# Optimization experiments

Hardware: AMD Instinct MI355X
Metric: run time of the kernel (lower is better)

The kernel has to match this reference:

```python
import jax, jax.numpy as jnp
import numpy as np

B, N, NVT, HS, NZ = 512, 256, 32, 128, 64


def setup_inputs() -> dict:
    key = jax.random.key(0)
    ks = jax.random.split(key, 16)
    node_types = jax.random.randint(ks[0], (B, N), 0, NVT, dtype=jnp.int32)
    node_types = node_types.at[:, 0].set(0)      # START_TYPE
    node_types = node_types.at[:, -1].set(1)     # END_TYPE
    adj = jax.random.randint(ks[1], (B, N, N), 0, 2, dtype=jnp.int32)
    # DAG: edges only u -> v with u < v (strict upper triangular)
    tri = jnp.triu(jnp.ones((N, N), jnp.int32), k=1)
    adj = adj * tri[None, :, :]
    s = 0.05
    p = lambda k, shp: (jax.random.normal(k, shp, jnp.float32) * s)
    return {
        "node_types": node_types,
        "adj": adj,
        "W_ih": p(ks[2], (3 * HS, NVT)),   # grue_forward weight_ih
        "W_hh": p(ks[3], (3 * HS, HS)),    # grue_forward weight_hh
        "b_ih": p(ks[4], (3 * HS,)),
        "b_hh": p(ks[5], (3 * HS,)),
        "Wg": p(ks[6], (HS, NVT)),         # gate_forward linear
        "bg": p(ks[7], (HS,)),
        "Wm": p(ks[8], (HS, NVT)),         # mapper_forward (no bias)
        "W1": p(ks[9], (NZ, HS)),          # fc1 -> mu
        "b1": p(ks[10], (NZ,)),
        "W2": p(ks[11], (NZ, HS)),         # fc2 -> logvar
        "b2": p(ks[12], (NZ,)),
    }


def reference(node_types, adj, W_ih, W_hh, b_ih, b_hh, Wg, bg, Wm, W1, b1, W2, b2):
    hs = Wg.shape[0]
    # one-hot vertex types  [B, N, nvt]
    X = jax.nn.one_hot(node_types, Wg.shape[1], dtype=W_ih.dtype)
    # gated message from each vertex's TYPE (mapper has no bias -> padding contributes 0)
    gated = jax.nn.sigmoid(jnp.einsum('bnv,hv->bnh', X, Wg) + bg) \
            * jnp.einsum('bnv,hv->bnh', X, Wm)                      # [B, N, hs]
    A = adj.astype(gated.dtype)
    # predecessor aggregation: H_v = sum_{u: u->v} gated_u
    Hpre = jnp.einsum('buv,buh->bvh', A, gated)                     # [B, N, hs]
    # torch GRUCell(X_v, Hpre_v), vectorized over all vertices (no recurrence:
    # messages depend only on predecessor types)
    gi = jnp.einsum('bnv,gv->bng', X, W_ih) + b_ih                  # [B, N, 3hs]
    gh = jnp.einsum('bnh,gh->bng', Hpre, W_hh) + b_hh
    r = jax.nn.sigmoid(gi[..., :hs] + gh[..., :hs])
    z = jax.nn.sigmoid(gi[..., hs:2 * hs] + gh[..., hs:2 * hs])
    n = jnp.tanh(gi[..., 2 * hs:] + r * gh[..., 2 * hs:])
    Hv = (1.0 - z) * n + z * Hpre                                   # H_forward, [B, N, hs]
    # graph state: sum over vertices [1, N-1) (start=1, end_offset=1)
    Hg = Hv[:, 1:-1, :].sum(axis=1)                                 # [B, hs]
    mu = Hg @ W1.T + b1
    logvar = Hg @ W2.T + b2
    return (mu, logvar)
```

## Files before the change

### kernel.cpp

```cpp
#include <hip/hip_runtime.h>
#include <hip/hip_bf16.h>

#define HS 128
#define NVT 32
#define NN 256

typedef __attribute__((ext_vector_type(8))) short bf16x8;
typedef __attribute__((ext_vector_type(4))) short s16x4;
typedef __attribute__((ext_vector_type(4))) float f32x4;

#define TABB_OFF 0
#define GIT2_OFF 32768

static __device__ __forceinline__ short f2bs(float f) {
    __hip_bfloat16 h = __float2bfloat16(f);
    short s; __builtin_memcpy(&s, &h, 2);
    return s;
}
static __device__ __forceinline__ float bs2f(short s) {
    __hip_bfloat16 h; __builtin_memcpy(&h, &s, 2);
    return __bfloat162float(h);
}
static __device__ __forceinline__ float sigm(float x) {
    return __builtin_amdgcn_rcpf(1.f + __expf(-x));
}

__global__ void __launch_bounds__(512) build_tables(
    const float* __restrict__ W_ih, const float* __restrict__ W_hh,
    const float* __restrict__ b_ih, const float* __restrict__ b_hh,
    const float* __restrict__ Wg,   const float* __restrict__ bg,
    const float* __restrict__ Wm,
    short* __restrict__ TABB, short* __restrict__ GIT2)
{
    __shared__ float G_s[HS];
    const int t = blockIdx.x;
    const int j = threadIdx.x;
    if (j < HS) {
        float x = Wg[j * NVT + t] + bg[j];
        G_s[j] = sigm(x) * Wm[j * NVT + t];
    }
    __syncthreads();
    if (j < 384) {
        float acc = 0.f;
        for (int h = 0; h < HS; ++h) acc += G_s[h] * W_hh[j * HS + h];
        TABB[j * NVT + t] = f2bs(acc);
        float git = W_ih[j * NVT + t] + b_ih[j];
        int gate = j >> 7, h = j & 127;
        if (gate < 2) git += b_hh[j];
        GIT2[(t * 128 + h) * 4 + gate] = f2bs(git);
    } else {
        TABB[j * NVT + t] = f2bs(G_s[j - 384]);
        GIT2[(t * 128 + (j - 384)) * 4 + 3] = 0;
    }
}

__global__ void __launch_bounds__(256) dvae_fused(
    const int* __restrict__ node_types, const int* __restrict__ adj,
    const short* __restrict__ TABB, const short* __restrict__ GIT2,
    const float* __restrict__ b_hh,
    const float* __restrict__ W1, const float* __restrict__ b1,
    const float* __restrict__ W2, const float* __restrict__ b2,
    float* __restrict__ out)
{
    __shared__ unsigned cntA[NN * 20];
    __shared__ short GITs[NVT * 512];
    __shared__ unsigned pc[4 * NN * 8];
    __shared__ unsigned tmask[NVT * 8];
    __shared__ int types_s[NN];
    __shared__ float hg_s[HS];

    const int b = blockIdx.x, tid = threadIdx.x;
    const int wave = tid >> 6, lane = tid & 63;
    const int quad = lane >> 4, col = lane & 15;

    types_s[tid] = node_types[b * NN + tid];

    {
        const uint4* src = (const uint4*)GIT2;
        uint4* dst = (uint4*)GITs;
        #pragma unroll
        for (int i = 0; i < 8; ++i) dst[i * 256 + tid] = src[i * 256 + tid];
    }
    bf16x8 bfrag[8];
    #pragma unroll
    for (int i = 0; i < 8; ++i) {
        int gate = i >> 1, sub = (i & 1) * 16;
        int jb = (gate < 3 ? gate * 128 : 384) + wave * 32 + sub;
        bfrag[i] = *(const bf16x8*)(TABB + (jb + col) * 32 + quad * 8);
    }
    const int h0 = wave * 32 + col;
    const float bhn0 = b_hh[256 + h0], bhn1 = b_hh[256 + h0 + 16];
    __syncthreads();

    {
        int t = tid >> 3, w8 = tid & 7;
        const int* ty = types_s + w8 * 32;
        unsigned mw = 0;
        #pragma unroll
        for (int k = 0; k < 32; ++k) mw |= ((unsigned)(ty[k] == t)) << k;
        tmask[tid] = mw;
    }

    const uint4* adjb = (const uint4*)(adj + (size_t)b * NN * NN) + wave * 64 * 64 + lane;
    unsigned cb0a = 0, cb0b = 0, cb1a = 0, cb1b = 0, cb2a = 0, cb2b = 0, cb3a = 0, cb3b = 0;
    #pragma unroll
    for (int half = 0; half < 2; ++half) {
        #pragma unroll
        for (int bb = 0; bb < 4; ++bb) {
            uint4 av[8];
            #pragma unroll
            for (int j = 0; j < 8; ++j) av[j] = adjb[(half * 32 + bb * 8 + j) * 64];
            #pragma unroll
            for (int j = 0; j < 8; ++j) {
                int sh = bb * 8 + j;
                if (half == 0) {
                    cb0a |= av[j].x << sh; cb1a |= av[j].y << sh;
                    cb2a |= av[j].z << sh; cb3a |= av[j].w << sh;
                } else {
                    cb0b |= av[j].x << sh; cb1b |= av[j].y << sh;
                    cb2b |= av[j].z << sh; cb3b |= av[j].w << sh;
                }
            }
        }
    }
    __syncthreads();

    unsigned pcnt[4][8];
    #pragma unroll
    for (int k = 0; k < 4; ++k)
        #pragma unroll
        for (int q = 0; q < 8; ++q) pcnt[k][q] = 0;
    #pragma unroll
    for (int t = 0; t < 32; ++t) {
        unsigned tm0 = tmask[t * 8 + wave * 2];
        unsigned tm1 = tmask[t * 8 + wave * 2 + 1];
        unsigned sh = (unsigned)((t & 3) * 8);
        pcnt[0][t >> 2] += (__popc(cb0a & tm0) + __popc(cb0b & tm1)) << sh;
        pcnt[1][t >> 2] += (__popc(cb1a & tm0) + __popc(cb1b & tm1)) << sh;
        pcnt[2][t >> 2] += (__popc(cb2a & tm0) + __popc(cb2b & tm1)) << sh;
        pcnt[3][t >> 2] += (__popc(cb3a & tm0) + __popc(cb3b & tm1)) << sh;
    }
    {
        uint4* p4 = (uint4*)pc;
        #pragma unroll
        for (int k = 0; k < 4; ++k) {
            int c = lane * 4 + k;
            p4[(wave * NN + c) * 2]     = make_uint4(pcnt[k][0], pcnt[k][1], pcnt[k][2], pcnt[k][3]);
            p4[(wave * NN + c) * 2 + 1] = make_uint4(pcnt[k][4], pcnt[k][5], pcnt[k][6], pcnt[k][7]);
        }
    }
    __syncthreads();

    {
        #pragma unroll
        for (int q = 0; q < 8; ++q) {
            unsigned u = pc[(0 * NN + tid) * 8 + q] + pc[(1 * NN + tid) * 8 + q]
                       + pc[(2 * NN + tid) * 8 + q] + pc[(3 * NN + tid) * 8 + q];
            float f0 = (float)(u & 0xFF),         f1 = (float)((u >> 8) & 0xFF);
            float f2 = (float)((u >> 16) & 0xFF), f3 = (float)((u >> 24) & 0xFF);
            cntA[tid * 20 + 2 * q]     = (__float_as_uint(f0) >> 16) | (__float_as_uint(f1) & 0xFFFF0000u);
            cntA[tid * 20 + 2 * q + 1] = (__float_as_uint(f2) >> 16) | (__float_as_uint(f3) & 0xFFFF0000u);
        }
    }
    __syncthreads();

    float hg0 = 0.f, hg1 = 0.f;
    for (int m = 0; m < 16; ++m) {
        bf16x8 afrag = *(const bf16x8*)(cntA + (m * 16 + col) * 20 + quad * 4);
        f32x4 acc[8];
        #pragma unroll
        for (int i = 0; i < 8; ++i)
            acc[i] = __builtin_amdgcn_mfma_f32_16x16x32_bf16(
                afrag, bfrag[i], (f32x4){0.f, 0.f, 0.f, 0.f}, 0, 0, 0);
        #pragma unroll
        for (int r = 0; r < 4; ++r) {
            int vv = m * 16 + quad * 4 + r;
            int tv = types_s[vv];
            float msk = (vv >= 1 && vv < NN - 1) ? 1.f : 0.f;
            {
                s16x4 gg = *(const s16x4*)(GITs + (tv * 128 + h0) * 4);
                float rr = sigm(bs2f(gg[0]) + acc[0][r]);
                float zz = sigm(bs2f(gg[1]) + acc[2][r]);
                float x2 = bs2f(gg[2]) + rr * (acc[4][r] + bhn0);
                float nt = 1.f - 2.f * __builtin_amdgcn_rcpf(1.f + __expf(2.f * x2));
                hg0 += msk * ((1.f - zz) * nt + zz * acc[6][r]);
            }
            {
                s16x4 gg = *(const s16x4*)(GITs + (tv * 128 + h0 + 16) * 4);
                float rr = sigm(bs2f(gg[0]) + acc[1][r]);
                float zz = sigm(bs2f(gg[1]) + acc[3][r]);
                float x2 = bs2f(gg[2]) + rr * (acc[5][r] + bhn1);
                float nt = 1.f - 2.f * __builtin_amdgcn_rcpf(1.f + __expf(2.f * x2));
                hg1 += msk * ((1.f - zz) * nt + zz * acc[7][r]);
            }
        }
    }
    hg0 += __shfl_xor(hg0, 16); hg0 += __shfl_xor(hg0, 32);
    hg1 += __shfl_xor(hg1, 16); hg1 += __shfl_xor(hg1, 32);
    if (lane < 16) { hg_s[h0] = hg0; hg_s[h0 + 16] = hg1; }
    __syncthreads();

    if (tid < 128) {
        int which = tid >> 6, zz = tid & 63;
        const float* W = which ? W2 : W1;
        float acc2 = which ? b2[zz] : b1[zz];
        const float4* Wv = (const float4*)(W + zz * HS);
        #pragma unroll
        for (int i = 0; i < 32; ++i) {
            float4 ww = Wv[i];
            acc2 += hg_s[4 * i] * ww.x + hg_s[4 * i + 1] * ww.y
                  + hg_s[4 * i + 2] * ww.z + hg_s[4 * i + 3] * ww.w;
        }
        out[which * 32768 + b * 64 + zz] = acc2;
    }
}

extern "C" void kernel_launch(void* const* d_in, const int* in_sizes, int n_in,
                              void* d_out, int out_size, void* d_ws, size_t ws_size,
                              hipStream_t stream)
{
    const int* node_types = (const int*)d_in[0];
    const int* adj        = (const int*)d_in[1];
    const float* W_ih = (const float*)d_in[2];
    const float* W_hh = (const float*)d_in[3];
    const float* b_ih = (const float*)d_in[4];
    const float* b_hh = (const float*)d_in[5];
    const float* Wg   = (const float*)d_in[6];
    const float* bg   = (const float*)d_in[7];
    const float* Wm   = (const float*)d_in[8];
    const float* W1   = (const float*)d_in[9];
    const float* b1   = (const float*)d_in[10];
    const float* W2   = (const float*)d_in[11];
    const float* b2   = (const float*)d_in[12];

    char* ws = (char*)d_ws;
    short* TABB = (short*)(ws + TABB_OFF);
    short* GIT2 = (short*)(ws + GIT2_OFF);
    float* out  = (float*)d_out;

    build_tables<<<dim3(32), dim3(512), 0, stream>>>(W_ih, W_hh, b_ih, b_hh, Wg, bg, Wm, TABB, GIT2);
    dvae_fused<<<dim3(512), dim3(256), 0, stream>>>(node_types, adj, TABB, GIT2, b_hh, W1, b1, W2, b2, out);
}
```

Before: 251.2 us.

## Split adjacency histogram into separate kernel using direct global-to-LDS loads

New measurement: 246.0 us. 2.1% less time.

```diff
diff --git a/kernel.cpp b/kernel.cpp
--- a/kernel.cpp
+++ b/kernel.cpp
@@ -11,6 +11,7 @@
 
 #define TABB_OFF 0
 #define GIT2_OFF 32768
+#define CNT_OFF  65536
 
 static __device__ __forceinline__ short f2bs(float f) {
     __hip_bfloat16 h = __float2bfloat16(f);
@@ -23,6 +24,11 @@
 }
 static __device__ __forceinline__ float sigm(float x) {
     return __builtin_amdgcn_rcpf(1.f + __expf(-x));
+}
+static __device__ __forceinline__ void lds_load16(const void* g, void* l) {
+    __builtin_amdgcn_global_load_lds(
+        (const __attribute__((address_space(1))) unsigned int*)g,
+        (__attribute__((address_space(3))) unsigned int*)l, 16, 0, 0);
 }
 
 __global__ void __launch_bounds__(512) build_tables(
@@ -54,8 +60,65 @@
     }
 }
 
-__global__ void __launch_bounds__(256) dvae_fused(
+__global__ void __launch_bounds__(256) hist(
     const int* __restrict__ node_types, const int* __restrict__ adj,
+    unsigned* __restrict__ cnt_out)
+{
+    __shared__ int tile[64 * NN];
+    __shared__ unsigned tmask[NVT * 8];
+    __shared__ int types_s[NN];
+
+    const int b = blockIdx.x, tid = threadIdx.x;
+    const int wave = tid >> 6, lane = tid & 63;
+
+    types_s[tid] = node_types[b * NN + tid];
+    __syncthreads();
+    {
+        int t = tid >> 3, w8 = tid & 7;
+        const int* ty = types_s + w8 * 32;
+        unsigned mw = 0;
+        #pragma unroll
+        for (int k = 0; k < 32; ++k) mw |= ((unsigned)(ty[k] == t)) << k;
+        tmask[tid] = mw;
+    }
+
+    const char* gb = (const char*)(adj + (size_t)b * NN * NN);
+    unsigned pcnt[8] = {0, 0, 0, 0, 0, 0, 0, 0};
+
+    for (int tk = 0; tk < 4; ++tk) {
+        #pragma unroll
+        for (int j = 0; j < 16; ++j) {
+            int r = wave * 16 + j;
+            lds_load16(gb + (size_t)(tk * 64 + r) * 1024 + lane * 16, &tile[r * NN]);
+        }
+        __syncthreads();
+        unsigned w0 = 0, w1 = 0;
+        #pragma unroll
+        for (int rr = 0; rr < 32; ++rr) w0 |= ((unsigned)tile[rr * NN + tid]) << rr;
+        #pragma unroll
+        for (int rr = 0; rr < 32; ++rr) w1 |= ((unsigned)tile[(32 + rr) * NN + tid]) << rr;
+        #pragma unroll
+        for (int t = 0; t < NVT; ++t) {
+            unsigned c = __popc(w0 & tmask[t * 8 + 2 * tk])
+                       + __popc(w1 & tmask[t * 8 + 2 * tk + 1]);
+            pcnt[t >> 2] += c << ((t & 3) * 8);
+        }
+        __syncthreads();
+    }
+
+    unsigned* dst = cnt_out + ((size_t)b * NN + tid) * 16;
+    #pragma unroll
+    for (int q = 0; q < 8; ++q) {
+        unsigned u = pcnt[q];
+        float f0 = (float)(u & 0xFF),         f1 = (float)((u >> 8) & 0xFF);
+        float f2 = (float)((u >> 16) & 0xFF), f3 = (float)((u >> 24) & 0xFF);
+        dst[2 * q]     = (__float_as_uint(f0) >> 16) | (__float_as_uint(f1) & 0xFFFF0000u);
+        dst[2 * q + 1] = (__float_as_uint(f2) >> 16) | (__float_as_uint(f3) & 0xFFFF0000u);
+    }
+}
+
+__global__ void __launch_bounds__(256) dvae_main(
+    const int* __restrict__ node_types, const unsigned* __restrict__ cntw,
     const short* __restrict__ TABB, const short* __restrict__ GIT2,
     const float* __restrict__ b_hh,
     const float* __restrict__ W1, const float* __restrict__ b1,
@@ -64,8 +127,6 @@
 {
     __shared__ unsigned cntA[NN * 20];
     __shared__ short GITs[NVT * 512];
-    __shared__ unsigned pc[4 * NN * 8];
-    __shared__ unsigned tmask[NVT * 8];
     __shared__ int types_s[NN];
     __shared__ float hg_s[HS];
 
@@ -75,6 +136,12 @@
 
     types_s[tid] = node_types[b * NN + tid];
 
+    {
+        const uint4* src = (const uint4*)(cntw + ((size_t)b * NN + tid) * 16);
+        uint4* drow = (uint4*)(cntA + tid * 20);
+        #pragma unroll
+        for (int c = 0; c < 4; ++c) drow[c] = src[c];
+    }
     {
         const uint4* src = (const uint4*)GIT2;
         uint4* dst = (uint4*)GITs;
@@ -90,81 +157,9 @@
     }
     const int h0 = wave * 32 + col;
     const float bhn0 = b_hh[256 + h0], bhn1 = b_hh[256 + h0 + 16];
-    __syncthreads();
-
-    {
-        int t = tid >> 3, w8 = tid & 7;
-        const int* ty = types_s + w8 * 32;
-        unsigned mw = 0;
-        #pragma unroll
-        for (int k = 0; k < 32; ++k) mw |= ((unsigned)(ty[k] == t)) << k;
-        tmask[tid] = mw;
-    }
-
-    const uint4* adjb = (const uint4*)(adj + (size_t)b * NN * NN) + wave * 64 * 64 + lane;
-    unsigned cb0a = 0, cb0b = 0, cb1a = 0, cb1b = 0, cb2a = 0, cb2b = 0, cb3a = 0, cb3b = 0;
-    #pragma unroll
-    for (int half = 0; half < 2; ++half) {
-        #pragma unroll
-        for (int bb = 0; bb < 4; ++bb) {
-            uint4 av[8];
-            #pragma unroll
-            for (int j = 0; j < 8; ++j) av[j] = adjb[(half * 32 + bb * 8 + j) * 64];
-            #pragma unroll
-            for (int j = 0; j < 8; ++j) {
-                int sh = bb * 8 + j;
-                if (half == 0) {
-                    cb0a |= av[j].x << sh; cb1a |= av[j].y << sh;
-                    cb2a |= av[j].z << sh; cb3a |= av[j].w << sh;
-                } else {
-                    cb0b |= av[j].x << sh; cb1b |= av[j].y << sh;
-                    cb2b |= av[j].z << sh; cb3b |= av[j].w << sh;
-                }
-            }
-        }
-    }
-    __syncthreads();
-
-    unsigned pcnt[4][8];
-    #pragma unroll
-    for (int k = 0; k < 4; ++k)
-        #pragma unroll
-        for (int q = 0; q < 8; ++q) pcnt[k][q] = 0;
-    #pragma unroll
-    for (int t = 0; t < 32; ++t) {
-        unsigned tm0 = tmask[t * 8 + wave * 2];
-        unsigned tm1 = tmask[t * 8 + wave * 2 + 1];
-        unsigned sh = (unsigned)((t & 3) * 8);
-        pcnt[0][t >> 2] += (__popc(cb0a & tm0) + __popc(cb0b & tm1)) << sh;
-        pcnt[1][t >> 2] += (__popc(cb1a & tm0) + __popc(cb1b & tm1)) << sh;
-        pcnt[2][t >> 2] += (__popc(cb2a & tm0) + __popc(cb2b & tm1)) << sh;
-        pcnt[3][t >> 2] += (__popc(cb3a & tm0) + __popc(cb3b & tm1)) << sh;
-    }
-    {
-        uint4* p4 = (uint4*)pc;
-        #pragma unroll
-        for (int k = 0; k < 4; ++k) {
-            int c = lane * 4 + k;
-            p4[(wave * NN + c) * 2]     = make_uint4(pcnt[k][0], pcnt[k][1], pcnt[k][2], pcnt[k][3]);
-            p4[(wave * NN + c) * 2 + 1] = make_uint4(pcnt[k][4], pcnt[k][5], pcnt[k][6], pcnt[k][7]);
-        }
-    }
-    __syncthreads();
-
-    {
-        #pragma unroll
-        for (int q = 0; q < 8; ++q) {
-            unsigned u = pc[(0 * NN + tid) * 8 + q] + pc[(1 * NN + tid) * 8 + q]
-                       + pc[(2 * NN + tid) * 8 + q] + pc[(3 * NN + tid) * 8 + q];
-            float f0 = (float)(u & 0xFF),         f1 = (float)((u >> 8) & 0xFF);
-            float f2 = (float)((u >> 16) & 0xFF), f3 = (float)((u >> 24) & 0xFF);
-            cntA[tid * 20 + 2 * q]     = (__float_as_uint(f0) >> 16) | (__float_as_uint(f1) & 0xFFFF0000u);
-            cntA[tid * 20 + 2 * q + 1] = (__float_as_uint(f2) >> 16) | (__float_as_uint(f3) & 0xFFFF0000u);
-        }
-    }
-    __syncthreads();
-
     float hg0 = 0.f, hg1 = 0.f;
+    __syncthreads();
+
     for (int m = 0; m < 16; ++m) {
         bf16x8 afrag = *(const bf16x8*)(cntA + (m * 16 + col) * 20 + quad * 4);
         f32x4 acc[8];
@@ -236,8 +231,10 @@
     char* ws = (char*)d_ws;
     short* TABB = (short*)(ws + TABB_OFF);
     short* GIT2 = (short*)(ws + GIT2_OFF);
+    unsigned* cnt = (unsigned*)(ws + CNT_OFF);
     float* out  = (float*)d_out;
 
     build_tables<<<dim3(32), dim3(512), 0, stream>>>(W_ih, W_hh, b_ih, b_hh, Wg, bg, Wm, TABB, GIT2);
-    dvae_fused<<<dim3(512), dim3(256), 0, stream>>>(node_types, adj, TABB, GIT2, b_hh, W1, b1, W2, b2, out);
-}
+    hist<<<dim3(512), dim3(256), 0, stream>>>(node_types, adj, cnt);
+    dvae_main<<<dim3(512), dim3(256), 0, stream>>>(node_types, cnt, TABB, GIT2, b_hh, W1, b1, W2, b2, out);
+}
```
